# Performance work log

Hardware: AMD Instinct MI355X
Metric: run time of the kernel (lower is better)

Reference implementation:

```python
import jax, jax.numpy as jnp
import numpy as np

FEATURE_DIM = 4
LOSS_WEIGHT = 1.0
DELTA_V = 0.5
DELTA_D = 1.5
NUM_LABELS = 8  # instance ids 0..7; 0 = background
B, H, W = 16, 640, 640


def _safe_norm(x, axis):
    # L2 norm with grad-safe sqrt (forward value exact: 0 when sum of squares is 0)
    sq = jnp.sum(x * x, axis=axis)
    pos = sq > 0
    return jnp.where(pos, jnp.sqrt(jnp.where(pos, sq, 1.0)), 0.0)


def _single_loss(emb, instance, kernel, training_mask):
    # emb: [H,W,C], instance: [H,W] int, kernel/training_mask: [H,W] float
    C = emb.shape[-1]
    L = NUM_LABELS
    tm = training_mask > 0.5
    kr = kernel > 0.5
    inst = jnp.where(tm, instance, 0).reshape(-1)          # [P]
    inst_k = jnp.where(kr.reshape(-1), inst, 0)            # [P]
    emb_f = emb.reshape(-1, C)                              # [P,C]

    # per-label kernel-region means (emb_mean), label 0 column is zeros
    sums = jax.ops.segment_sum(emb_f, inst_k, num_segments=L)                       # [L,C]
    cnts = jax.ops.segment_sum(jnp.ones(inst_k.shape, jnp.float32), inst_k, L)      # [L]
    mu = sums / jnp.maximum(cnts, 1.0)[:, None]
    mu = mu.at[0].set(0.0)

    # aggregation term: per-pixel distance to its instance mean
    d = _safe_norm(emb_f - mu[inst], axis=1)                                         # [P]
    term = jnp.log(jnp.maximum(d - DELTA_V, 0.0) ** 2 + 1.0)
    cnt_i = jax.ops.segment_sum(jnp.ones(inst.shape, jnp.float32), inst, L)
    agg = jax.ops.segment_sum(term, inst, L) / jnp.maximum(cnt_i, 1.0)               # [L]
    # original skips label 0, then takes mean of l_agg[1:] -> drops first nonzero label
    l_agg = jnp.mean(agg[2:])

    # discrimination term: all ordered pairs of distinct nonzero labels
    dd = _safe_norm(mu[:, None, :] - mu[None, :, :], axis=-1)                        # [L,L]
    valid = (1.0 - jnp.eye(L, dtype=jnp.float32)).at[0, :].set(0.0).at[:, 0].set(0.0)
    dis = jnp.log(jnp.maximum(2.0 * DELTA_D - dd, 0.0) ** 2 + 1.0)
    l_dis = jnp.sum(dis * valid) / jnp.sum(valid)

    l_reg = jnp.mean(jnp.log(_safe_norm(mu, axis=1) + 1.0)) * 0.001
    return l_agg + l_dis + l_reg


def reference(emb, instance, kernel, training_mask):
    losses = jax.vmap(_single_loss)(emb, instance, kernel, training_mask)  # [B]
    return LOSS_WEIGHT * jnp.mean(losses)


def setup_inputs() -> dict:
    key = jax.random.key(0)
    k1, k2, k3 = jax.random.split(key, 3)
    emb = jax.random.normal(k1, (B, H, W, FEATURE_DIM), dtype=jnp.float32)
    instance = jax.random.randint(k2, (B, H, W), 0, NUM_LABELS, dtype=jnp.int32)
    kernel = jax.random.uniform(k3, (B, H, W), dtype=jnp.float32)
    training_mask = jnp.ones((B, H, W), dtype=jnp.float32)
    return {"emb": emb, "instance": instance, "kernel": kernel, "training_mask": training_mask}
```

## Files before the change

### kernel.cpp

```cpp
#include <hip/hip_runtime.h>
#include <math.h>

#define NLAB 8
#define BATCH 16
#define S_OFF  0
#define CK_OFF 28
#define CI_OFF 35
#define AG_OFF 41
#define ACC_PER_B 48
#define CNT_IDX (BATCH * ACC_PER_B)
#define ACC_ZERO_BYTES ((CNT_IDX + 1) * 4)
#define LAB_OFFSET 4096
#define GRID_X 64

__device__ __forceinline__ float wave_reduce(float v) {
#pragma unroll
  for (int off = 32; off > 0; off >>= 1) v += __shfl_xor(v, off, 64);
  return v;
}

__global__ __launch_bounds__(256, 4) void k_accum(
    const float4* __restrict__ emb, const int* __restrict__ inst,
    const float* __restrict__ ker, const float* __restrict__ tmk,
    float* __restrict__ acc, unsigned char* __restrict__ labc,
    int P, int use_cache)
{
  const int b = blockIdx.y;
  const size_t base = (size_t)b * P;
  const float4* e  = emb + base;
  const int*    ip = inst + base;
  const float*  kp = ker + base;
  const float*  tp = tmk + base;
  unsigned char* lb = labc + base;

  float s[28];
#pragma unroll
  for (int k = 0; k < 28; ++k) s[k] = 0.f;
  int ck[7] = {0, 0, 0, 0, 0, 0, 0};
  int ci[6] = {0, 0, 0, 0, 0, 0};

  const int lane = threadIdx.x & 63;
  const int wid  = threadIdx.x >> 6;
  const int ntiles = P >> 10;

  for (int t = blockIdx.x; t < ntiles; t += gridDim.x) {
    const int p0 = (t << 10) + (wid << 8) + lane;
    float4 e0 = e[p0];
    float4 e1 = e[p0 + 64];
    float4 e2 = e[p0 + 128];
    float4 e3 = e[p0 + 192];
    int   v0 = ip[p0], v1 = ip[p0 + 64], v2 = ip[p0 + 128], v3 = ip[p0 + 192];
    float q0 = kp[p0], q1 = kp[p0 + 64], q2 = kp[p0 + 128], q3 = kp[p0 + 192];
    float u0 = tp[p0], u1 = tp[p0 + 64], u2 = tp[p0 + 128], u3 = tp[p0 + 192];

    int lab0 = (u0 > 0.5f) ? (v0 & 7) : 0;
    int lab1 = (u1 > 0.5f) ? (v1 & 7) : 0;
    int lab2 = (u2 > 0.5f) ? (v2 & 7) : 0;
    int lab3 = (u3 > 0.5f) ? (v3 & 7) : 0;
    if (use_cache) {
      lb[p0]       = (unsigned char)lab0;
      lb[p0 + 64]  = (unsigned char)lab1;
      lb[p0 + 128] = (unsigned char)lab2;
      lb[p0 + 192] = (unsigned char)lab3;
    }
    int lk0 = (q0 > 0.5f) ? lab0 : 8;
    int lk1 = (q1 > 0.5f) ? lab1 : 8;
    int lk2 = (q2 > 0.5f) ? lab2 : 8;
    int lk3 = (q3 > 0.5f) ? lab3 : 8;

#pragma unroll
    for (int l = 1; l < NLAB; ++l) {
      bool h0 = (lk0 == l), h1 = (lk1 == l), h2 = (lk2 == l), h3 = (lk3 == l);
      ck[l - 1] += __popcll(__ballot(h0)) + __popcll(__ballot(h1)) +
                   __popcll(__ballot(h2)) + __popcll(__ballot(h3));
      float m0 = h0 ? 1.f : 0.f, m1 = h1 ? 1.f : 0.f;
      float m2 = h2 ? 1.f : 0.f, m3 = h3 ? 1.f : 0.f;
      const int o = (l - 1) * 4;
      s[o + 0] = fmaf(m0, e0.x, fmaf(m1, e1.x, fmaf(m2, e2.x, fmaf(m3, e3.x, s[o + 0]))));
      s[o + 1] = fmaf(m0, e0.y, fmaf(m1, e1.y, fmaf(m2, e2.y, fmaf(m3, e3.y, s[o + 1]))));
      s[o + 2] = fmaf(m0, e0.z, fmaf(m1, e1.z, fmaf(m2, e2.z, fmaf(m3, e3.z, s[o + 2]))));
      s[o + 3] = fmaf(m0, e0.w, fmaf(m1, e1.w, fmaf(m2, e2.w, fmaf(m3, e3.w, s[o + 3]))));
    }
#pragma unroll
    for (int l = 2; l < NLAB; ++l) {
      ci[l - 2] += __popcll(__ballot(lab0 == l)) + __popcll(__ballot(lab1 == l)) +
                   __popcll(__ballot(lab2 == l)) + __popcll(__ballot(lab3 == l));
    }
  }

  if (blockIdx.x == 0) {
    for (int p = (ntiles << 10) + (int)threadIdx.x; p < P; p += (int)blockDim.x) {
      int lab = (tp[p] > 0.5f) ? (ip[p] & 7) : 0;
      float kr = kp[p];
      float4 ev = e[p];
      if (lab >= 1 && kr > 0.5f) {
        atomicAdd(&acc[b * ACC_PER_B + (lab - 1) * 4 + 0], ev.x);
        atomicAdd(&acc[b * ACC_PER_B + (lab - 1) * 4 + 1], ev.y);
        atomicAdd(&acc[b * ACC_PER_B + (lab - 1) * 4 + 2], ev.z);
        atomicAdd(&acc[b * ACC_PER_B + (lab - 1) * 4 + 3], ev.w);
        atomicAdd(&acc[b * ACC_PER_B + CK_OFF + lab - 1], 1.f);
      }
      if (lab >= 2) atomicAdd(&acc[b * ACC_PER_B + CI_OFF + lab - 2], 1.f);
    }
  }

#pragma unroll
  for (int off = 32; off > 0; off >>= 1) {
    float tsh[28];
#pragma unroll
    for (int k = 0; k < 28; ++k) tsh[k] = __shfl_xor(s[k], off, 64);
#pragma unroll
    for (int k = 0; k < 28; ++k) s[k] += tsh[k];
  }

  __shared__ float redf[4][28];
  __shared__ int   redi[4][13];
  if (lane == 0) {
#pragma unroll
    for (int k = 0; k < 28; ++k) redf[wid][k] = s[k];
#pragma unroll
    for (int k = 0; k < 7; ++k) redi[wid][k] = ck[k];
#pragma unroll
    for (int k = 0; k < 6; ++k) redi[wid][7 + k] = ci[k];
  }
  __syncthreads();
  if (threadIdx.x < 28) {
    float v = redf[0][threadIdx.x] + redf[1][threadIdx.x] +
              redf[2][threadIdx.x] + redf[3][threadIdx.x];
    atomicAdd(acc + b * ACC_PER_B + S_OFF + threadIdx.x, v);
  } else if (threadIdx.x >= 32 && threadIdx.x < 32 + 13) {
    int j = threadIdx.x - 32;
    int v = redi[0][j] + redi[1][j] + redi[2][j] + redi[3][j];
    atomicAdd(acc + b * ACC_PER_B + CK_OFF + j, (float)v);
  }
}

__global__ __launch_bounds__(256, 4) void k_agg(
    const float4* __restrict__ emb, const int* __restrict__ inst,
    const float* __restrict__ tmk, const unsigned char* __restrict__ labc,
    float* __restrict__ acc, float* __restrict__ out,
    int P, int use_cache, int nblocks)
{
  const int b = blockIdx.y;
  const size_t base = (size_t)b * P;
  __shared__ float4 smu[NLAB];
  const float* accB = acc + b * ACC_PER_B;
  if (threadIdx.x < NLAB) {
    int l = threadIdx.x;
    float4 m = make_float4(0.f, 0.f, 0.f, 0.f);
    if (l > 0) {
      float inv = 1.f / fmaxf(accB[CK_OFF + l - 1], 1.f);
      m = make_float4(accB[S_OFF + (l - 1) * 4 + 0] * inv,
                      accB[S_OFF + (l - 1) * 4 + 1] * inv,
                      accB[S_OFF + (l - 1) * 4 + 2] * inv,
                      accB[S_OFF + (l - 1) * 4 + 3] * inv);
    }
    smu[l] = m;
  }
  __syncthreads();

  const float4* e = emb + base;
  const int*    ip = inst + base;
  const float*  tp = tmk + base;
  const unsigned char* lb = labc + base;

  float ag[6] = {0.f, 0.f, 0.f, 0.f, 0.f, 0.f};
  const int lane = threadIdx.x & 63;
  const int wid  = threadIdx.x >> 6;
  const int ntiles = P >> 10;

  for (int t = blockIdx.x; t < ntiles; t += gridDim.x) {
    const int p0 = (t << 10) + (wid << 8) + lane;
    int lab0, lab1, lab2, lab3;
    if (use_cache) {
      lab0 = lb[p0]; lab1 = lb[p0 + 64]; lab2 = lb[p0 + 128]; lab3 = lb[p0 + 192];
    } else {
      lab0 = (tp[p0] > 0.5f)       ? (ip[p0] & 7)       : 0;
      lab1 = (tp[p0 + 64] > 0.5f)  ? (ip[p0 + 64] & 7)  : 0;
      lab2 = (tp[p0 + 128] > 0.5f) ? (ip[p0 + 128] & 7) : 0;
      lab3 = (tp[p0 + 192] > 0.5f) ? (ip[p0 + 192] & 7) : 0;
    }
    float4 e0 = e[p0];
    float4 e1 = e[p0 + 64];
    float4 e2 = e[p0 + 128];
    float4 e3 = e[p0 + 192];

#pragma unroll
    for (int i = 0; i < 4; ++i) {
      int lab = (i == 0) ? lab0 : (i == 1) ? lab1 : (i == 2) ? lab2 : lab3;
      float4 ev = (i == 0) ? e0 : (i == 1) ? e1 : (i == 2) ? e2 : e3;
      float4 mv = smu[lab];
      float dx = ev.x - mv.x, dy = ev.y - mv.y;
      float dz = ev.z - mv.z, dw = ev.w - mv.w;
      float sq = dx * dx + dy * dy + dz * dz + dw * dw;
      float d = sqrtf(sq);
      float tt = fmaxf(d - 0.5f, 0.f);
      float term = logf(fmaf(tt, tt, 1.f));
#pragma unroll
      for (int l = 0; l < 6; ++l) ag[l] += (lab == l + 2) ? term : 0.f;
    }
  }

  if (blockIdx.x == 0) {
    for (int p = (ntiles << 10) + (int)threadIdx.x; p < P; p += (int)blockDim.x) {
      int lab = (tp[p] > 0.5f) ? (ip[p] & 7) : 0;
      if (lab >= 2) {
        float4 ev = e[p]; float4 mv = smu[lab];
        float dx = ev.x - mv.x, dy = ev.y - mv.y;
        float dz = ev.z - mv.z, dw = ev.w - mv.w;
        float d = sqrtf(dx * dx + dy * dy + dz * dz + dw * dw);
        float tt = fmaxf(d - 0.5f, 0.f);
        atomicAdd(&acc[b * ACC_PER_B + AG_OFF + lab - 2], logf(fmaf(tt, tt, 1.f)));
      }
    }
  }

#pragma unroll
  for (int off = 32; off > 0; off >>= 1) {
    float tsh[6];
#pragma unroll
    for (int k = 0; k < 6; ++k) tsh[k] = __shfl_xor(ag[k], off, 64);
#pragma unroll
    for (int k = 0; k < 6; ++k) ag[k] += tsh[k];
  }
  __shared__ float redf[4][6];
  if (lane == 0) {
#pragma unroll
    for (int k = 0; k < 6; ++k) redf[wid][k] = ag[k];
  }
  __syncthreads();
  if (threadIdx.x < 6) {
    float v = redf[0][threadIdx.x] + redf[1][threadIdx.x] +
              redf[2][threadIdx.x] + redf[3][threadIdx.x];
    atomicAdd(acc + b * ACC_PER_B + AG_OFF + threadIdx.x, v);
  }

  __syncthreads();
  __shared__ int amlast;
  if (threadIdx.x == 0) {
    __threadfence();
    unsigned int* cnt = (unsigned int*)(acc + CNT_IDX);
    unsigned int old = atomicAdd(cnt, 1u);
    amlast = (old == (unsigned int)(nblocks - 1)) ? 1 : 0;
  }
  __syncthreads();
  if (amlast && threadIdx.x < 64) {
    __threadfence();
    float loss = 0.f;
    if (threadIdx.x < BATCH) {
      const float* a = acc + threadIdx.x * ACC_PER_B;
      float av[47];
#pragma unroll
      for (int k = 0; k < 47; ++k)
        av[k] = __hip_atomic_load(&a[k], __ATOMIC_RELAXED, __HIP_MEMORY_SCOPE_AGENT);
      float mu[NLAB][4];
#pragma unroll
      for (int c = 0; c < 4; ++c) mu[0][c] = 0.f;
#pragma unroll
      for (int l = 1; l < NLAB; ++l) {
        float inv = 1.f / fmaxf(av[CK_OFF + l - 1], 1.f);
#pragma unroll
        for (int c = 0; c < 4; ++c) mu[l][c] = av[S_OFF + (l - 1) * 4 + c] * inv;
      }
      float l_agg = 0.f;
#pragma unroll
      for (int l = 2; l < NLAB; ++l)
        l_agg += av[AG_OFF + l - 2] / fmaxf(av[CI_OFF + l - 2], 1.f);
      l_agg *= (1.f / 6.f);
      float ssum = 0.f;
      for (int i = 1; i < NLAB; ++i)
        for (int j = 1; j < NLAB; ++j) {
          if (i == j) continue;
          float dx = mu[i][0] - mu[j][0], dy = mu[i][1] - mu[j][1];
          float dz = mu[i][2] - mu[j][2], dw = mu[i][3] - mu[j][3];
          float dd = sqrtf(dx * dx + dy * dy + dz * dz + dw * dw);
          float tt = fmaxf(3.0f - dd, 0.f);
          ssum += logf(fmaf(tt, tt, 1.f));
        }
      float l_dis = ssum / 42.f;
      float rsum = 0.f;
#pragma unroll
      for (int l = 1; l < NLAB; ++l) {
        float n = sqrtf(mu[l][0] * mu[l][0] + mu[l][1] * mu[l][1] +
                        mu[l][2] * mu[l][2] + mu[l][3] * mu[l][3]);
        rsum += logf(n + 1.f);
      }
      float l_reg = rsum * (0.001f / NLAB);
      loss = l_agg + l_dis + l_reg;
    }
    loss = wave_reduce(loss);
    if (threadIdx.x == 0) out[0] = loss * (1.f / BATCH);
  }
}

extern "C" void kernel_launch(void* const* d_in, const int* in_sizes, int n_in,
                              void* d_out, int out_size, void* d_ws, size_t ws_size,
                              hipStream_t stream) {
  const float4* emb  = (const float4*)d_in[0];
  const int*    inst = (const int*)d_in[1];
  const float*  ker  = (const float*)d_in[2];
  const float*  tmk  = (const float*)d_in[3];
  float* out = (float*)d_out;

  const int total = in_sizes[1];
  const int P = total / BATCH;

  float* acc = (float*)d_ws;
  unsigned char* labc = (unsigned char*)d_ws + LAB_OFFSET;
  const size_t need = (size_t)LAB_OFFSET + (size_t)total;
  const int use_cache = (ws_size >= need) ? 1 : 0;

  hipMemsetAsync(d_ws, 0, ACC_ZERO_BYTES, stream);

  dim3 grid(GRID_X, BATCH);
  k_accum<<<grid, 256, 0, stream>>>(emb, inst, ker, tmk, acc, labc, P, use_cache);
  k_agg  <<<grid, 256, 0, stream>>>(emb, inst, tmk, labc, acc, out, P, use_cache,
                                    GRID_X * BATCH);
}
```

Before: 272.3 us.

## Software-pipeline tile loads in accum and agg kernels with double buffering

New measurement: 299.2 us. 1.1x slower.

```diff
diff --git a/kernel.cpp b/kernel.cpp
--- a/kernel.cpp
+++ b/kernel.cpp
@@ -19,6 +19,72 @@
   return v;
 }
 
+
+struct AccTile {
+  float4 e0, e1, e2, e3;
+  int    v0, v1, v2, v3;
+  float  q0, q1, q2, q3;
+  float  u0, u1, u2, u3;
+  int    p0;
+};
+
+__device__ __forceinline__ AccTile acc_issue(
+    const float4* __restrict__ e, const int* __restrict__ ip,
+    const float* __restrict__ kp, const float* __restrict__ tp,
+    int t, int wid, int lane)
+{
+  AccTile T;
+  T.p0 = (t << 10) + (wid << 8) + lane;
+  T.e0 = e[T.p0];       T.e1 = e[T.p0 + 64];
+  T.e2 = e[T.p0 + 128]; T.e3 = e[T.p0 + 192];
+  T.v0 = ip[T.p0];       T.v1 = ip[T.p0 + 64];
+  T.v2 = ip[T.p0 + 128]; T.v3 = ip[T.p0 + 192];
+  T.q0 = kp[T.p0];       T.q1 = kp[T.p0 + 64];
+  T.q2 = kp[T.p0 + 128]; T.q3 = kp[T.p0 + 192];
+  T.u0 = tp[T.p0];       T.u1 = tp[T.p0 + 64];
+  T.u2 = tp[T.p0 + 128]; T.u3 = tp[T.p0 + 192];
+  return T;
+}
+
+__device__ __forceinline__ void acc_process(
+    const AccTile& T, unsigned char* __restrict__ lb, int use_cache,
+    float (&s)[28], int (&ck)[7], int (&ci)[6])
+{
+  int lab0 = (T.u0 > 0.5f) ? (T.v0 & 7) : 0;
+  int lab1 = (T.u1 > 0.5f) ? (T.v1 & 7) : 0;
+  int lab2 = (T.u2 > 0.5f) ? (T.v2 & 7) : 0;
+  int lab3 = (T.u3 > 0.5f) ? (T.v3 & 7) : 0;
+  if (use_cache) {
+    lb[T.p0]       = (unsigned char)lab0;
+    lb[T.p0 + 64]  = (unsigned char)lab1;
+    lb[T.p0 + 128] = (unsigned char)lab2;
+    lb[T.p0 + 192] = (unsigned char)lab3;
+  }
+  int lk0 = (T.q0 > 0.5f) ? lab0 : 8;
+  int lk1 = (T.q1 > 0.5f) ? lab1 : 8;
+  int lk2 = (T.q2 > 0.5f) ? lab2 : 8;
+  int lk3 = (T.q3 > 0.5f) ? lab3 : 8;
+
+#pragma unroll
+  for (int l = 1; l < NLAB; ++l) {
+    bool h0 = (lk0 == l), h1 = (lk1 == l), h2 = (lk2 == l), h3 = (lk3 == l);
+    ck[l - 1] += __popcll(__ballot(h0)) + __popcll(__ballot(h1)) +
+                 __popcll(__ballot(h2)) + __popcll(__ballot(h3));
+    float m0 = h0 ? 1.f : 0.f, m1 = h1 ? 1.f : 0.f;
+    float m2 = h2 ? 1.f : 0.f, m3 = h3 ? 1.f : 0.f;
+    const int o = (l - 1) * 4;
+    s[o + 0] = fmaf(m0, T.e0.x, fmaf(m1, T.e1.x, fmaf(m2, T.e2.x, fmaf(m3, T.e3.x, s[o + 0]))));
+    s[o + 1] = fmaf(m0, T.e0.y, fmaf(m1, T.e1.y, fmaf(m2, T.e2.y, fmaf(m3, T.e3.y, s[o + 1]))));
+    s[o + 2] = fmaf(m0, T.e0.z, fmaf(m1, T.e1.z, fmaf(m2, T.e2.z, fmaf(m3, T.e3.z, s[o + 2]))));
+    s[o + 3] = fmaf(m0, T.e0.w, fmaf(m1, T.e1.w, fmaf(m2, T.e2.w, fmaf(m3, T.e3.w, s[o + 3]))));
+  }
+#pragma unroll
+  for (int l = 2; l < NLAB; ++l) {
+    ci[l - 2] += __popcll(__ballot(lab0 == l)) + __popcll(__ballot(lab1 == l)) +
+                 __popcll(__ballot(lab2 == l)) + __popcll(__ballot(lab3 == l));
+  }
+}
+
 __global__ __launch_bounds__(256, 4) void k_accum(
     const float4* __restrict__ emb, const int* __restrict__ inst,
     const float* __restrict__ ker, const float* __restrict__ tmk,
@@ -42,49 +108,21 @@
   const int lane = threadIdx.x & 63;
   const int wid  = threadIdx.x >> 6;
   const int ntiles = P >> 10;
-
-  for (int t = blockIdx.x; t < ntiles; t += gridDim.x) {
-    const int p0 = (t << 10) + (wid << 8) + lane;
-    float4 e0 = e[p0];
-    float4 e1 = e[p0 + 64];
-    float4 e2 = e[p0 + 128];
-    float4 e3 = e[p0 + 192];
-    int   v0 = ip[p0], v1 = ip[p0 + 64], v2 = ip[p0 + 128], v3 = ip[p0 + 192];
-    float q0 = kp[p0], q1 = kp[p0 + 64], q2 = kp[p0 + 128], q3 = kp[p0 + 192];
-    float u0 = tp[p0], u1 = tp[p0 + 64], u2 = tp[p0 + 128], u3 = tp[p0 + 192];
-
-    int lab0 = (u0 > 0.5f) ? (v0 & 7) : 0;
-    int lab1 = (u1 > 0.5f) ? (v1 & 7) : 0;
-    int lab2 = (u2 > 0.5f) ? (v2 & 7) : 0;
-    int lab3 = (u3 > 0.5f) ? (v3 & 7) : 0;
-    if (use_cache) {
-      lb[p0]       = (unsigned char)lab0;
-      lb[p0 + 64]  = (unsigned char)lab1;
-      lb[p0 + 128] = (unsigned char)lab2;
-      lb[p0 + 192] = (unsigned char)lab3;
-    }
-    int lk0 = (q0 > 0.5f) ? lab0 : 8;
-    int lk1 = (q1 > 0.5f) ? lab1 : 8;
-    int lk2 = (q2 > 0.5f) ? lab2 : 8;
-    int lk3 = (q3 > 0.5f) ? lab3 : 8;
-
-#pragma unroll
-    for (int l = 1; l < NLAB; ++l) {
-      bool h0 = (lk0 == l), h1 = (lk1 == l), h2 = (lk2 == l), h3 = (lk3 == l);
-      ck[l - 1] += __popcll(__ballot(h0)) + __popcll(__ballot(h1)) +
-                   __popcll(__ballot(h2)) + __popcll(__ballot(h3));
-      float m0 = h0 ? 1.f : 0.f, m1 = h1 ? 1.f : 0.f;
-      float m2 = h2 ? 1.f : 0.f, m3 = h3 ? 1.f : 0.f;
-      const int o = (l - 1) * 4;
-      s[o + 0] = fmaf(m0, e0.x, fmaf(m1, e1.x, fmaf(m2, e2.x, fmaf(m3, e3.x, s[o + 0]))));
-      s[o + 1] = fmaf(m0, e0.y, fmaf(m1, e1.y, fmaf(m2, e2.y, fmaf(m3, e3.y, s[o + 1]))));
-      s[o + 2] = fmaf(m0, e0.z, fmaf(m1, e1.z, fmaf(m2, e2.z, fmaf(m3, e3.z, s[o + 2]))));
-      s[o + 3] = fmaf(m0, e0.w, fmaf(m1, e1.w, fmaf(m2, e2.w, fmaf(m3, e3.w, s[o + 3]))));
-    }
-#pragma unroll
-    for (int l = 2; l < NLAB; ++l) {
-      ci[l - 2] += __popcll(__ballot(lab0 == l)) + __popcll(__ballot(lab1 == l)) +
-                   __popcll(__ballot(lab2 == l)) + __popcll(__ballot(lab3 == l));
+  const int stride = gridDim.x;
+
+  int t = blockIdx.x;
+  if (t < ntiles) {
+    AccTile A = acc_issue(e, ip, kp, tp, t, wid, lane);
+    for (;;) {
+      int tB = t + stride;
+      if (tB >= ntiles) { acc_process(A, lb, use_cache, s, ck, ci); break; }
+      AccTile Bt = acc_issue(e, ip, kp, tp, tB, wid, lane);
+      acc_process(A, lb, use_cache, s, ck, ci);
+      int tA = tB + stride;
+      if (tA >= ntiles) { acc_process(Bt, lb, use_cache, s, ck, ci); break; }
+      A = acc_issue(e, ip, kp, tp, tA, wid, lane);
+      acc_process(Bt, lb, use_cache, s, ck, ci);
+      t = tA;
     }
   }
 
@@ -135,6 +173,58 @@
   }
 }
 
+
+struct AggTile {
+  float4 e0, e1, e2, e3;
+  int    l0, l1, l2, l3;
+  int    v0, v1, v2, v3;
+  float  u0, u1, u2, u3;
+  int    p0;
+};
+
+__device__ __forceinline__ AggTile agg_issue(
+    const float4* __restrict__ e, const unsigned char* __restrict__ lb,
+    const int* __restrict__ ip, const float* __restrict__ tp,
+    int t, int wid, int lane, int use_cache)
+{
+  AggTile T;
+  T.p0 = (t << 10) + (wid << 8) + lane;
+  T.e0 = e[T.p0];       T.e1 = e[T.p0 + 64];
+  T.e2 = e[T.p0 + 128]; T.e3 = e[T.p0 + 192];
+  if (use_cache) {
+    T.l0 = lb[T.p0];       T.l1 = lb[T.p0 + 64];
+    T.l2 = lb[T.p0 + 128]; T.l3 = lb[T.p0 + 192];
+  } else {
+    T.v0 = ip[T.p0];       T.v1 = ip[T.p0 + 64];
+    T.v2 = ip[T.p0 + 128]; T.v3 = ip[T.p0 + 192];
+    T.u0 = tp[T.p0];       T.u1 = tp[T.p0 + 64];
+    T.u2 = tp[T.p0 + 128]; T.u3 = tp[T.p0 + 192];
+  }
+  return T;
+}
+
+__device__ __forceinline__ void agg_process(
+    const AggTile& T, const float4 (&smu)[NLAB], int use_cache, float (&ag)[6])
+{
+  int lab0 = use_cache ? T.l0 : ((T.u0 > 0.5f) ? (T.v0 & 7) : 0);
+  int lab1 = use_cache ? T.l1 : ((T.u1 > 0.5f) ? (T.v1 & 7) : 0);
+  int lab2 = use_cache ? T.l2 : ((T.u2 > 0.5f) ? (T.v2 & 7) : 0);
+  int lab3 = use_cache ? T.l3 : ((T.u3 > 0.5f) ? (T.v3 & 7) : 0);
+#pragma unroll
+  for (int i = 0; i < 4; ++i) {
+    int lab = (i == 0) ? lab0 : (i == 1) ? lab1 : (i == 2) ? lab2 : lab3;
+    float4 ev = (i == 0) ? T.e0 : (i == 1) ? T.e1 : (i == 2) ? T.e2 : T.e3;
+    float4 mv = smu[lab];
+    float dx = ev.x - mv.x, dy = ev.y - mv.y;
+    float dz = ev.z - mv.z, dw = ev.w - mv.w;
+    float d = sqrtf(dx * dx + dy * dy + dz * dz + dw * dw);
+    float tt = fmaxf(d - 0.5f, 0.f);
+    float term = logf(fmaf(tt, tt, 1.f));
+#pragma unroll
+    for (int l = 0; l < 6; ++l) ag[l] += (lab == l + 2) ? term : 0.f;
+  }
+}
+
 __global__ __launch_bounds__(256, 4) void k_agg(
     const float4* __restrict__ emb, const int* __restrict__ inst,
     const float* __restrict__ tmk, const unsigned char* __restrict__ labc,
@@ -143,7 +233,7 @@
 {
   const int b = blockIdx.y;
   const size_t base = (size_t)b * P;
-  __shared__ float4 smu[NLAB];
+  __shared__ float4 smu_s[NLAB];
   const float* accB = acc + b * ACC_PER_B;
   if (threadIdx.x < NLAB) {
     int l = threadIdx.x;
@@ -155,9 +245,12 @@
                       accB[S_OFF + (l - 1) * 4 + 2] * inv,
                       accB[S_OFF + (l - 1) * 4 + 3] * inv);
     }
-    smu[l] = m;
-  }
-  __syncthreads();
+    smu_s[l] = m;
+  }
+  __syncthreads();
+  float4 smu[NLAB];
+#pragma unroll
+  for (int l = 0; l < NLAB; ++l) smu[l] = smu_s[l];
 
   const float4* e = emb + base;
   const int*    ip = inst + base;
@@ -168,36 +261,21 @@
   const int lane = threadIdx.x & 63;
   const int wid  = threadIdx.x >> 6;
   const int ntiles = P >> 10;
-
-  for (int t = blockIdx.x; t < ntiles; t += gridDim.x) {
-    const int p0 = (t << 10) + (wid << 8) + lane;
-    int lab0, lab1, lab2, lab3;
-    if (use_cache) {
-      lab0 = lb[p0]; lab1 = lb[p0 + 64]; lab2 = lb[p0 + 128]; lab3 = lb[p0 + 192];
-    } else {
-      lab0 = (tp[p0] > 0.5f)       ? (ip[p0] & 7)       : 0;
-      lab1 = (tp[p0 + 64] > 0.5f)  ? (ip[p0 + 64] & 7)  : 0;
-      lab2 = (tp[p0 + 128] > 0.5f) ? (ip[p0 + 128] & 7) : 0;
-      lab3 = (tp[p0 + 192] > 0.5f) ? (ip[p0 + 192] & 7) : 0;
-    }
-    float4 e0 = e[p0];
-    float4 e1 = e[p0 + 64];
-    float4 e2 = e[p0 + 128];
-    float4 e3 = e[p0 + 192];
-
-#pragma unroll
-    for (int i = 0; i < 4; ++i) {
-      int lab = (i == 0) ? lab0 : (i == 1) ? lab1 : (i == 2) ? lab2 : lab3;
-      float4 ev = (i == 0) ? e0 : (i == 1) ? e1 : (i == 2) ? e2 : e3;
-      float4 mv = smu[lab];
-      float dx = ev.x - mv.x, dy = ev.y - mv.y;
-      float dz = ev.z - mv.z, dw = ev.w - mv.w;
-      float sq = dx * dx + dy * dy + dz * dz + dw * dw;
-      float d = sqrtf(sq);
-      float tt = fmaxf(d - 0.5f, 0.f);
-      float term = logf(fmaf(tt, tt, 1.f));
-#pragma unroll
-      for (int l = 0; l < 6; ++l) ag[l] += (lab == l + 2) ? term : 0.f;
+  const int stride = gridDim.x;
+
+  int t = blockIdx.x;
+  if (t < ntiles) {
+    AggTile A = agg_issue(e, lb, ip, tp, t, wid, lane, use_cache);
+    for (;;) {
+      int tB = t + stride;
+      if (tB >= ntiles) { agg_process(A, smu, use_cache, ag); break; }
+      AggTile Bt = agg_issue(e, lb, ip, tp, tB, wid, lane, use_cache);
+      agg_process(A, smu, use_cache, ag);
+      int tA = tB + stride;
+      if (tA >= ntiles) { agg_process(Bt, smu, use_cache, ag); break; }
+      A = agg_issue(e, lb, ip, tp, tA, wid, lane, use_cache);
+      agg_process(Bt, smu, use_cache, ag);
+      t = tA;
     }
   }
 
@@ -238,14 +316,13 @@
   __syncthreads();
   __shared__ int amlast;
   if (threadIdx.x == 0) {
-    __threadfence();
     unsigned int* cnt = (unsigned int*)(acc + CNT_IDX);
-    unsigned int old = atomicAdd(cnt, 1u);
+    unsigned int old = __hip_atomic_fetch_add(cnt, 1u, __ATOMIC_ACQ_REL,
+                                              __HIP_MEMORY_SCOPE_AGENT);
     amlast = (old == (unsigned int)(nblocks - 1)) ? 1 : 0;
   }
   __syncthreads();
   if (amlast && threadIdx.x < 64) {
-    __threadfence();
     float loss = 0.f;
     if (threadIdx.x < BATCH) {
       const float* a = acc + threadIdx.x * ACC_PER_B;
```

## Double-buffer global-to-LDS DMA loads in both kernels with per-wave chunking

Applied to the files above, without the earlier changes.

After: 288.0 us. +5.8%, slower.

```diff
diff --git a/kernel.cpp b/kernel.cpp
--- a/kernel.cpp
+++ b/kernel.cpp
@@ -11,7 +11,8 @@
 #define CNT_IDX (BATCH * ACC_PER_B)
 #define ACC_ZERO_BYTES ((CNT_IDX + 1) * 4)
 #define LAB_OFFSET 4096
-#define GRID_X 64
+#define GX_ACC 32
+#define GX_AGG 48
 
 __device__ __forceinline__ float wave_reduce(float v) {
 #pragma unroll
@@ -19,19 +20,35 @@
   return v;
 }
 
-__global__ __launch_bounds__(256, 4) void k_accum(
+__device__ __forceinline__ void dma16(const void* g, void* l) {
+  __builtin_amdgcn_global_load_lds((const __attribute__((address_space(1))) void*)g,
+                                   (__attribute__((address_space(3))) void*)l,
+                                   16, 0, 0);
+}
+__device__ __forceinline__ void dma4(const void* g, void* l) {
+  __builtin_amdgcn_global_load_lds((const __attribute__((address_space(1))) void*)g,
+                                   (__attribute__((address_space(3))) void*)l,
+                                   4, 0, 0);
+}
+
+
+__global__ __launch_bounds__(256, 2) void k_accum(
     const float4* __restrict__ emb, const int* __restrict__ inst,
     const float* __restrict__ ker, const float* __restrict__ tmk,
-    float* __restrict__ acc, unsigned char* __restrict__ labc,
+    float* __restrict__ acc, unsigned int* __restrict__ labc32,
     int P, int use_cache)
 {
+  __shared__ __align__(16) unsigned char lds[4][2][7168];
   const int b = blockIdx.y;
   const size_t base = (size_t)b * P;
-  const float4* e  = emb + base;
-  const int*    ip = inst + base;
-  const float*  kp = ker + base;
-  const float*  tp = tmk + base;
-  unsigned char* lb = labc + base;
+  const char* ge = (const char*)(emb + base);
+  const char* gi = (const char*)(inst + base);
+  const char* gk = (const char*)(ker + base);
+  const char* gt = (const char*)(tmk + base);
+  unsigned int* lb32 = labc32 + (base >> 2);
+
+  const int lane = threadIdx.x & 63;
+  const int wid  = threadIdx.x >> 6;
 
   float s[28];
 #pragma unroll
@@ -39,59 +56,84 @@
   int ck[7] = {0, 0, 0, 0, 0, 0, 0};
   int ci[6] = {0, 0, 0, 0, 0, 0};
 
-  const int lane = threadIdx.x & 63;
-  const int wid  = threadIdx.x >> 6;
-  const int ntiles = P >> 10;
-
-  for (int t = blockIdx.x; t < ntiles; t += gridDim.x) {
-    const int p0 = (t << 10) + (wid << 8) + lane;
-    float4 e0 = e[p0];
-    float4 e1 = e[p0 + 64];
-    float4 e2 = e[p0 + 128];
-    float4 e3 = e[p0 + 192];
-    int   v0 = ip[p0], v1 = ip[p0 + 64], v2 = ip[p0 + 128], v3 = ip[p0 + 192];
-    float q0 = kp[p0], q1 = kp[p0 + 64], q2 = kp[p0 + 128], q3 = kp[p0 + 192];
-    float u0 = tp[p0], u1 = tp[p0 + 64], u2 = tp[p0 + 128], u3 = tp[p0 + 192];
-
-    int lab0 = (u0 > 0.5f) ? (v0 & 7) : 0;
-    int lab1 = (u1 > 0.5f) ? (v1 & 7) : 0;
-    int lab2 = (u2 > 0.5f) ? (v2 & 7) : 0;
-    int lab3 = (u3 > 0.5f) ? (v3 & 7) : 0;
-    if (use_cache) {
-      lb[p0]       = (unsigned char)lab0;
-      lb[p0 + 64]  = (unsigned char)lab1;
-      lb[p0 + 128] = (unsigned char)lab2;
-      lb[p0 + 192] = (unsigned char)lab3;
-    }
-    int lk0 = (q0 > 0.5f) ? lab0 : 8;
-    int lk1 = (q1 > 0.5f) ? lab1 : 8;
-    int lk2 = (q2 > 0.5f) ? lab2 : 8;
-    int lk3 = (q3 > 0.5f) ? lab3 : 8;
-
-#pragma unroll
-    for (int l = 1; l < NLAB; ++l) {
-      bool h0 = (lk0 == l), h1 = (lk1 == l), h2 = (lk2 == l), h3 = (lk3 == l);
-      ck[l - 1] += __popcll(__ballot(h0)) + __popcll(__ballot(h1)) +
-                   __popcll(__ballot(h2)) + __popcll(__ballot(h3));
-      float m0 = h0 ? 1.f : 0.f, m1 = h1 ? 1.f : 0.f;
-      float m2 = h2 ? 1.f : 0.f, m3 = h3 ? 1.f : 0.f;
-      const int o = (l - 1) * 4;
-      s[o + 0] = fmaf(m0, e0.x, fmaf(m1, e1.x, fmaf(m2, e2.x, fmaf(m3, e3.x, s[o + 0]))));
-      s[o + 1] = fmaf(m0, e0.y, fmaf(m1, e1.y, fmaf(m2, e2.y, fmaf(m3, e3.y, s[o + 1]))));
-      s[o + 2] = fmaf(m0, e0.z, fmaf(m1, e1.z, fmaf(m2, e2.z, fmaf(m3, e3.z, s[o + 2]))));
-      s[o + 3] = fmaf(m0, e0.w, fmaf(m1, e1.w, fmaf(m2, e2.w, fmaf(m3, e3.w, s[o + 3]))));
-    }
-#pragma unroll
-    for (int l = 2; l < NLAB; ++l) {
-      ci[l - 2] += __popcll(__ballot(lab0 == l)) + __popcll(__ballot(lab1 == l)) +
-                   __popcll(__ballot(lab2 == l)) + __popcll(__ballot(lab3 == l));
+  const int nch = P >> 8;
+  const int wgid = blockIdx.x * 4 + wid;
+  const int wstride = gridDim.x * 4;
+
+#define ACC_ISSUE(c, bb) do {                                              \
+    unsigned char* L = lds[wid][bb];                                       \
+    const char* gE = ge + ((size_t)(c) << 12) + lane * 16;                 \
+    dma16(gE,          L);                                                 \
+    dma16(gE + 1024,   L + 1024);                                          \
+    dma16(gE + 2048,   L + 2048);                                          \
+    dma16(gE + 3072,   L + 3072);                                          \
+    dma16(gi + ((size_t)(c) << 10) + lane * 16, L + 4096);                 \
+    dma16(gk + ((size_t)(c) << 10) + lane * 16, L + 5120);                 \
+    dma16(gt + ((size_t)(c) << 10) + lane * 16, L + 6144);                 \
+  } while (0)
+
+#define ACC_PROCESS(c, bb) do {                                            \
+    const unsigned char* L = lds[wid][bb];                                 \
+    int4   iv = ((const int4*)(L + 4096))[lane];                           \
+    float4 kv = ((const float4*)(L + 5120))[lane];                         \
+    float4 uv = ((const float4*)(L + 6144))[lane];                         \
+    float4 e0 = ((const float4*)L)[4 * lane + 0];                          \
+    float4 e1 = ((const float4*)L)[4 * lane + 1];                          \
+    float4 e2 = ((const float4*)L)[4 * lane + 2];                          \
+    float4 e3 = ((const float4*)L)[4 * lane + 3];                          \
+    int lab0 = (uv.x > 0.5f) ? (iv.x & 7) : 0;                             \
+    int lab1 = (uv.y > 0.5f) ? (iv.y & 7) : 0;                             \
+    int lab2 = (uv.z > 0.5f) ? (iv.z & 7) : 0;                             \
+    int lab3 = (uv.w > 0.5f) ? (iv.w & 7) : 0;                             \
+    if (use_cache)                                                         \
+      lb32[((c) << 6) + lane] = (unsigned)lab0 | ((unsigned)lab1 << 8) |   \
+                                ((unsigned)lab2 << 16) | ((unsigned)lab3 << 24); \
+    int lk0 = (kv.x > 0.5f) ? lab0 : 8;                                    \
+    int lk1 = (kv.y > 0.5f) ? lab1 : 8;                                    \
+    int lk2 = (kv.z > 0.5f) ? lab2 : 8;                                    \
+    int lk3 = (kv.w > 0.5f) ? lab3 : 8;                                    \
+    _Pragma("unroll")                                                      \
+    for (int l = 1; l < NLAB; ++l) {                                       \
+      bool h0 = (lk0 == l), h1 = (lk1 == l), h2 = (lk2 == l), h3 = (lk3 == l); \
+      ck[l - 1] += __popcll(__ballot(h0)) + __popcll(__ballot(h1)) +       \
+                   __popcll(__ballot(h2)) + __popcll(__ballot(h3));        \
+      float m0 = h0 ? 1.f : 0.f, m1 = h1 ? 1.f : 0.f;                      \
+      float m2 = h2 ? 1.f : 0.f, m3 = h3 ? 1.f : 0.f;                      \
+      const int o = (l - 1) * 4;                                           \
+      s[o + 0] = fmaf(m0, e0.x, fmaf(m1, e1.x, fmaf(m2, e2.x, fmaf(m3, e3.x, s[o + 0])))); \
+      s[o + 1] = fmaf(m0, e0.y, fmaf(m1, e1.y, fmaf(m2, e2.y, fmaf(m3, e3.y, s[o + 1])))); \
+      s[o + 2] = fmaf(m0, e0.z, fmaf(m1, e1.z, fmaf(m2, e2.z, fmaf(m3, e3.z, s[o + 2])))); \
+      s[o + 3] = fmaf(m0, e0.w, fmaf(m1, e1.w, fmaf(m2, e2.w, fmaf(m3, e3.w, s[o + 3])))); \
+    }                                                                      \
+    _Pragma("unroll")                                                      \
+    for (int l = 2; l < NLAB; ++l)                                         \
+      ci[l - 2] += __popcll(__ballot(lab0 == l)) + __popcll(__ballot(lab1 == l)) + \
+                   __popcll(__ballot(lab2 == l)) + __popcll(__ballot(lab3 == l));  \
+  } while (0)
+
+  if (wgid < nch) {
+    int cur = wgid, bufc = 0;
+    ACC_ISSUE(cur, 0);
+    for (;;) {
+      int nxt = cur + wstride;
+      if (nxt < nch) {
+        ACC_ISSUE(nxt, bufc ^ 1);
+        asm volatile("s_waitcnt vmcnt(7)" ::: "memory");
+        ACC_PROCESS(cur, bufc);
+        cur = nxt; bufc ^= 1;
+      } else {
+        asm volatile("s_waitcnt vmcnt(0)" ::: "memory");
+        ACC_PROCESS(cur, bufc);
+        break;
+      }
     }
   }
 
   if (blockIdx.x == 0) {
-    for (int p = (ntiles << 10) + (int)threadIdx.x; p < P; p += (int)blockDim.x) {
-      int lab = (tp[p] > 0.5f) ? (ip[p] & 7) : 0;
-      float kr = kp[p];
+    const float4* e = emb + base;
+    for (int p = (nch << 8) + (int)threadIdx.x; p < P; p += (int)blockDim.x) {
+      int lab = (tmk[base + p] > 0.5f) ? (inst[base + p] & 7) : 0;
+      float kr = ker[base + p];
       float4 ev = e[p];
       if (lab >= 1 && kr > 0.5f) {
         atomicAdd(&acc[b * ACC_PER_B + (lab - 1) * 4 + 0], ev.x);
@@ -135,15 +177,17 @@
   }
 }
 
-__global__ __launch_bounds__(256, 4) void k_agg(
+
+__global__ __launch_bounds__(256, 3) void k_agg(
     const float4* __restrict__ emb, const int* __restrict__ inst,
     const float* __restrict__ tmk, const unsigned char* __restrict__ labc,
     float* __restrict__ acc, float* __restrict__ out,
     int P, int use_cache, int nblocks)
 {
+  __shared__ __align__(16) unsigned char lds[4][2][6144];
   const int b = blockIdx.y;
   const size_t base = (size_t)b * P;
-  __shared__ float4 smu[NLAB];
+  __shared__ float4 smu_s[NLAB];
   const float* accB = acc + b * ACC_PER_B;
   if (threadIdx.x < NLAB) {
     int l = threadIdx.x;
@@ -155,55 +199,94 @@
                       accB[S_OFF + (l - 1) * 4 + 2] * inv,
                       accB[S_OFF + (l - 1) * 4 + 3] * inv);
     }
-    smu[l] = m;
+    smu_s[l] = m;
   }
   __syncthreads();
-
-  const float4* e = emb + base;
-  const int*    ip = inst + base;
-  const float*  tp = tmk + base;
-  const unsigned char* lb = labc + base;
-
-  float ag[6] = {0.f, 0.f, 0.f, 0.f, 0.f, 0.f};
+  float4 smu[NLAB];
+#pragma unroll
+  for (int l = 0; l < NLAB; ++l) smu[l] = smu_s[l];
+
+  const char* ge = (const char*)(emb + base);
+  const char* gi = (const char*)(inst + base);
+  const char* gt = (const char*)(tmk + base);
+  const unsigned char* gl = labc + base;
+
   const int lane = threadIdx.x & 63;
   const int wid  = threadIdx.x >> 6;
-  const int ntiles = P >> 10;
-
-  for (int t = blockIdx.x; t < ntiles; t += gridDim.x) {
-    const int p0 = (t << 10) + (wid << 8) + lane;
-    int lab0, lab1, lab2, lab3;
-    if (use_cache) {
-      lab0 = lb[p0]; lab1 = lb[p0 + 64]; lab2 = lb[p0 + 128]; lab3 = lb[p0 + 192];
-    } else {
-      lab0 = (tp[p0] > 0.5f)       ? (ip[p0] & 7)       : 0;
-      lab1 = (tp[p0 + 64] > 0.5f)  ? (ip[p0 + 64] & 7)  : 0;
-      lab2 = (tp[p0 + 128] > 0.5f) ? (ip[p0 + 128] & 7) : 0;
-      lab3 = (tp[p0 + 192] > 0.5f) ? (ip[p0 + 192] & 7) : 0;
-    }
-    float4 e0 = e[p0];
-    float4 e1 = e[p0 + 64];
-    float4 e2 = e[p0 + 128];
-    float4 e3 = e[p0 + 192];
-
-#pragma unroll
-    for (int i = 0; i < 4; ++i) {
-      int lab = (i == 0) ? lab0 : (i == 1) ? lab1 : (i == 2) ? lab2 : lab3;
-      float4 ev = (i == 0) ? e0 : (i == 1) ? e1 : (i == 2) ? e2 : e3;
-      float4 mv = smu[lab];
-      float dx = ev.x - mv.x, dy = ev.y - mv.y;
-      float dz = ev.z - mv.z, dw = ev.w - mv.w;
-      float sq = dx * dx + dy * dy + dz * dz + dw * dw;
-      float d = sqrtf(sq);
-      float tt = fmaxf(d - 0.5f, 0.f);
-      float term = logf(fmaf(tt, tt, 1.f));
-#pragma unroll
-      for (int l = 0; l < 6; ++l) ag[l] += (lab == l + 2) ? term : 0.f;
+
+  float ag[6] = {0.f, 0.f, 0.f, 0.f, 0.f, 0.f};
+  const int nch = P >> 8;
+  const int wgid = blockIdx.x * 4 + wid;
+  const int wstride = gridDim.x * 4;
+
+#define AGG_ISSUE(c, bb) do {                                              \
+    unsigned char* L = lds[wid][bb];                                       \
+    const char* gE = ge + ((size_t)(c) << 12) + lane * 16;                 \
+    dma16(gE,          L);                                                 \
+    dma16(gE + 1024,   L + 1024);                                          \
+    dma16(gE + 2048,   L + 2048);                                          \
+    dma16(gE + 3072,   L + 3072);                                          \
+    if (use_cache) {                                                       \
+      dma4(gl + ((size_t)(c) << 8) + lane * 4, L + 4096);                  \
+    } else {                                                               \
+      dma16(gi + ((size_t)(c) << 10) + lane * 16, L + 4096);               \
+      dma16(gt + ((size_t)(c) << 10) + lane * 16, L + 5120);               \
+    }                                                                      \
+  } while (0)
+
+#define AGG_PROCESS(c, bb) do {                                            \
+    const unsigned char* L = lds[wid][bb];                                 \
+    int lab0, lab1, lab2, lab3;                                            \
+    if (use_cache) {                                                       \
+      unsigned lw = ((const unsigned*)(L + 4096))[lane];                   \
+      lab0 = lw & 255; lab1 = (lw >> 8) & 255;                             \
+      lab2 = (lw >> 16) & 255; lab3 = (lw >> 24) & 255;                    \
+    } else {                                                               \
+      int4   iv = ((const int4*)(L + 4096))[lane];                         \
+      float4 uv = ((const float4*)(L + 5120))[lane];                       \
+      lab0 = (uv.x > 0.5f) ? (iv.x & 7) : 0;                               \
+      lab1 = (uv.y > 0.5f) ? (iv.y & 7) : 0;                               \
+      lab2 = (uv.z > 0.5f) ? (iv.z & 7) : 0;                               \
+      lab3 = (uv.w > 0.5f) ? (iv.w & 7) : 0;                               \
+    }                                                                      \
+    _Pragma("unroll")                                                      \
+    for (int j = 0; j < 4; ++j) {                                          \
+      int lab = (j == 0) ? lab0 : (j == 1) ? lab1 : (j == 2) ? lab2 : lab3;\
+      float4 ev = ((const float4*)L)[4 * lane + j];                        \
+      float4 mv = smu[lab];                                                \
+      float dx = ev.x - mv.x, dy = ev.y - mv.y;                            \
+      float dz = ev.z - mv.z, dw = ev.w - mv.w;                            \
+      float d = sqrtf(dx * dx + dy * dy + dz * dz + dw * dw);              \
+      float tt = fmaxf(d - 0.5f, 0.f);                        \
+      float term = logf(fmaf(tt, tt, 1.f));                                \
+      _Pragma("unroll")                                                    \
+      for (int l = 0; l < 6; ++l) ag[l] += (lab == l + 2) ? term : 0.f;    \
+    }                                                                      \
+  } while (0)
+
+  if (wgid < nch) {
+    int cur = wgid, bufc = 0;
+    AGG_ISSUE(cur, 0);
+    for (;;) {
+      int nxt = cur + wstride;
+      if (nxt < nch) {
+        AGG_ISSUE(nxt, bufc ^ 1);
+        if (use_cache) asm volatile("s_waitcnt vmcnt(5)" ::: "memory");
+        else           asm volatile("s_waitcnt vmcnt(6)" ::: "memory");
+        AGG_PROCESS(cur, bufc);
+        cur = nxt; bufc ^= 1;
+      } else {
+        asm volatile("s_waitcnt vmcnt(0)" ::: "memory");
+        AGG_PROCESS(cur, bufc);
+        break;
+      }
     }
   }
 
   if (blockIdx.x == 0) {
-    for (int p = (ntiles << 10) + (int)threadIdx.x; p < P; p += (int)blockDim.x) {
-      int lab = (tp[p] > 0.5f) ? (ip[p] & 7) : 0;
+    const float4* e = emb + base;
+    for (int p = (nch << 8) + (int)threadIdx.x; p < P; p += (int)blockDim.x) {
+      int lab = (tmk[base + p] > 0.5f) ? (inst[base + p] & 7) : 0;
       if (lab >= 2) {
         float4 ev = e[p]; float4 mv = smu[lab];
         float dx = ev.x - mv.x, dy = ev.y - mv.y;
@@ -238,14 +321,13 @@
   __syncthreads();
   __shared__ int amlast;
   if (threadIdx.x == 0) {
-    __threadfence();
     unsigned int* cnt = (unsigned int*)(acc + CNT_IDX);
-    unsigned int old = atomicAdd(cnt, 1u);
+    unsigned int old = __hip_atomic_fetch_add(cnt, 1u, __ATOMIC_ACQ_REL,
+                                              __HIP_MEMORY_SCOPE_AGENT);
     amlast = (old == (unsigned int)(nblocks - 1)) ? 1 : 0;
   }
   __syncthreads();
   if (amlast && threadIdx.x < 64) {
-    __threadfence();
     float loss = 0.f;
     if (threadIdx.x < BATCH) {
       const float* a = acc + threadIdx.x * ACC_PER_B;
@@ -308,12 +390,14 @@
   float* acc = (float*)d_ws;
   unsigned char* labc = (unsigned char*)d_ws + LAB_OFFSET;
   const size_t need = (size_t)LAB_OFFSET + (size_t)total;
-  const int use_cache = (ws_size >= need) ? 1 : 0;
+  const int use_cache = (ws_size >= need && (P & 3) == 0) ? 1 : 0;
 
   hipMemsetAsync(d_ws, 0, ACC_ZERO_BYTES, stream);
 
-  dim3 grid(GRID_X, BATCH);
-  k_accum<<<grid, 256, 0, stream>>>(emb, inst, ker, tmk, acc, labc, P, use_cache);
-  k_agg  <<<grid, 256, 0, stream>>>(emb, inst, tmk, labc, acc, out, P, use_cache,
-                                    GRID_X * BATCH);
-}
+  dim3 ga(GX_ACC, BATCH);
+  dim3 gb(GX_AGG, BATCH);
+  k_accum<<<ga, 256, 0, stream>>>(emb, inst, ker, tmk, acc,
+                                  (unsigned int*)labc, P, use_cache);
+  k_agg  <<<gb, 256, 0, stream>>>(emb, inst, tmk, labc, acc, out, P, use_cache,
+                                  GX_AGG * BATCH);
+}
```
